# Kernel tuning notes

Measured on AMD Instinct MI355X. Metric: run time of the kernel, lower is better.

Reference implementation:

```python
import jax, jax.numpy as jnp
import numpy as np

N = 100000        # nodes
E = 3200000       # edges (avg in-degree ~32)
NG = 64           # graphs in batch
F_IN = 64         # num_node_features
AVG_LOG = float(np.log(33.0))   # avg log-degree baked from deg (avg degree 32)
BN_EPS = 1e-5
STD_EPS = 1e-5

def _glorot(key, fi, fo):
    lim = float(np.sqrt(6.0 / (fi + fo)))
    return jax.random.uniform(key, (fi, fo), jnp.float32, -lim, lim)

def setup_inputs():
    key = jax.random.key(0)
    ks = jax.random.split(key, 16)
    inp = {
        'x': jax.random.normal(ks[0], (N, F_IN), jnp.float32),
        'edge_index': jax.random.randint(ks[1], (2, E), 0, N),
        'batch': jnp.sort(jax.random.randint(ks[2], (N,), 0, NG)),
    }
    dims = [(F_IN, 96), (96, 64), (64, 32), (32, 20)]
    for i, (fi, fo) in enumerate(dims):
        inp[f'w{i}'] = _glorot(ks[3 + i], 13 * fi, fo)  # (4 aggr * 3 scalers + 1 self) * F_in
        inp[f'b{i}'] = jnp.zeros((fo,), jnp.float32)
    for i, c in enumerate([96, 64, 20]):
        inp[f'g{i}'] = jnp.ones((c,), jnp.float32)
        inp[f'be{i}'] = jnp.zeros((c,), jnp.float32)
    inp['w_lin'] = _glorot(ks[10], 20, 11)
    inp['b_lin'] = jnp.zeros((11,), jnp.float32)
    return inp

def _pna_layer(x, src, dst, cnt, degc, W, b):
    m = x[src]                                          # [E, F] gather of neighbor feats
    inv = (1.0 / degc)[:, None]
    mean = jax.ops.segment_sum(m, dst, N) * inv
    mean_sq = jax.ops.segment_sum(m * m, dst, N) * inv
    std = jnp.sqrt(jax.nn.relu(mean_sq - mean * mean) + STD_EPS)
    has = (cnt > 0)[:, None]
    mn = jnp.where(has, jax.ops.segment_min(m, dst, N), 0.0)
    mx = jnp.where(has, jax.ops.segment_max(m, dst, N), 0.0)
    agg = jnp.concatenate([mean, mn, mx, std], axis=-1)  # [N, 4F]
    logd = jnp.log(degc + 1.0)[:, None]
    out = jnp.concatenate([agg, agg * (logd / AVG_LOG), agg * (AVG_LOG / logd)], axis=-1)  # [N, 12F]
    out = jnp.concatenate([x, out], axis=-1)             # [N, 13F] self + scaled aggregations
    return out @ W + b

def _bn(x, g, b):
    mu = x.mean(0)
    var = x.var(0)  # biased var: matches torch BatchNorm training forward
    return (x - mu) * jax.lax.rsqrt(var + BN_EPS) * g + b

def _forward(x, edge_index, batch, w0, b0, w1, b1, w2, b2, w3, b3,
             g0, be0, g1, be1, g2, be2, w_lin, b_lin):
    src, dst = edge_index[0], edge_index[1]
    cnt = jax.ops.segment_sum(jnp.ones((E,), x.dtype), dst, N)  # in-degree
    degc = jnp.maximum(cnt, 1.0)
    h = jax.nn.relu(_bn(_pna_layer(x, src, dst, cnt, degc, w0, b0), g0, be0))
    h = jax.nn.relu(_bn(_pna_layer(h, src, dst, cnt, degc, w1, b1), g1, be1))
    h = jax.nn.relu(_pna_layer(h, src, dst, cnt, degc, w2, b2))
    h = _bn(_pna_layer(h, src, dst, cnt, degc, w3, b3), g2, be2)
    gcnt = jnp.maximum(jax.ops.segment_sum(jnp.ones((N,), h.dtype), batch, NG), 1.0)
    z = jax.ops.segment_sum(h, batch, NG) / gcnt[:, None]       # global mean pool [NG, 20]
    out = jax.nn.softmax(z @ w_lin + b_lin, axis=-1)            # dropout identity (eval)
    return out, z

def reference(x, edge_index, batch, w0, b0, w1, b1, w2, b2, w3, b3,
              g0, be0, g1, be1, g2, be2, w_lin, b_lin):
    return _forward(x, edge_index, batch, w0, b0, w1, b1, w2, b2, w3, b3,
                    g0, be0, g1, be1, g2, be2, w_lin, b_lin)
```

## Files before the change

kernel.cpp:

```cpp
#include <hip/hip_runtime.h>

#define NN 100000
#define NGRAPH 64
#define NPART 8
#define NPB 12500
#define DB 16
#define PW_C 2048
#define AVGLOG 3.4965075614664802f

using f32x4 = __attribute__((ext_vector_type(4))) float;
using f16x8 = __attribute__((ext_vector_type(8))) _Float16;
using f16x4 = __attribute__((ext_vector_type(4))) _Float16;
using i32x4 = __attribute__((ext_vector_type(4))) int;

__global__ __launch_bounds__(256) void k_pcnt(const int* __restrict__ ei,
                                              int* __restrict__ pcnt, int E, int W) {
  const int w = blockIdx.x * 4 + (threadIdx.x >> 6);
  const int lane = threadIdx.x & 63;
  if (w >= W) return;
  int c[NPART];
#pragma unroll
  for (int b = 0; b < NPART; ++b) c[b] = 0;
  const long long base = (long long)w * PW_C;
  for (int r = 0; r < PW_C / 256; ++r) {
    long long e0 = base + r * 256 + lane * 4;
    int bk[4] = {-1, -1, -1, -1};
    if (e0 + 3 < E) {
      i32x4 d = __builtin_nontemporal_load((const i32x4*)(ei + E + e0));
#pragma unroll
      for (int k = 0; k < 4; ++k) bk[k] = d[k] / NPB;
    } else {
#pragma unroll
      for (int k = 0; k < 4; ++k)
        if (e0 + k < E) bk[k] = ei[E + e0 + k] / NPB;
    }
#pragma unroll
    for (int b = 0; b < NPART; ++b) {
      int t = 0;
#pragma unroll
      for (int k = 0; k < 4; ++k) t += __popcll(__ballot(bk[k] == b));
      c[b] += t;
    }
  }
  if (lane == 0) {
#pragma unroll
    for (int b = 0; b < NPART; ++b) pcnt[w * NPART + b] = c[b];
  }
}

__global__ void k_pscan(const int* __restrict__ pcnt, int* __restrict__ pbase,
                        int* __restrict__ bcur, int W) {
  __shared__ int s[256];
  __shared__ int btot[NPART];
  const int t = threadIdx.x;
  const int per = (W + 255) / 256;
  for (int b = 0; b < NPART; ++b) {
    int loc = 0;
    const int w0 = t * per;
    for (int i = 0; i < per; ++i) {
      int w = w0 + i;
      if (w < W) loc += pcnt[w * NPART + b];
    }
    s[t] = loc;
    __syncthreads();
    for (int off = 1; off < 256; off <<= 1) {
      int u = (t >= off) ? s[t - off] : 0;
      __syncthreads();
      s[t] += u;
      __syncthreads();
    }
    int run = s[t] - loc;
    if (t == 255) btot[b] = s[255];
    for (int i = 0; i < per; ++i) {
      int w = w0 + i;
      if (w < W) {
        pbase[w * NPART + b] = run;
        run += pcnt[w * NPART + b];
      }
    }
    __syncthreads();
  }
  if (t < NPART) bcur[t] = btot[t];
}

__global__ __launch_bounds__(256) void k_pbin(const int* __restrict__ ei,
                                              const int* __restrict__ pbase,
                                              unsigned long long* __restrict__ bkt,
                                              int cap, int E, int W) {
  const int w = blockIdx.x * 4 + (threadIdx.x >> 6);
  const int lane = threadIdx.x & 63;
  if (w >= W) return;
  int off[NPART];
#pragma unroll
  for (int b = 0; b < NPART; ++b) off[b] = pbase[w * NPART + b];
  const unsigned long long lmask = (1ull << lane) - 1ull;
  const long long base = (long long)w * PW_C;
  for (int r = 0; r < PW_C / 256; ++r) {
    long long e0 = base + r * 256 + lane * 4;
    int bk[4] = {-1, -1, -1, -1};
    int sv[4], dv[4];
    if (e0 + 3 < E) {
      i32x4 d = __builtin_nontemporal_load((const i32x4*)(ei + E + e0));
      i32x4 s4 = __builtin_nontemporal_load((const i32x4*)(ei + e0));
#pragma unroll
      for (int k = 0; k < 4; ++k) { dv[k] = d[k]; sv[k] = s4[k]; bk[k] = d[k] / NPB; }
    } else {
#pragma unroll
      for (int k = 0; k < 4; ++k)
        if (e0 + k < E) { dv[k] = ei[E + e0 + k]; sv[k] = ei[e0 + k]; bk[k] = dv[k] / NPB; }
    }
#pragma unroll
    for (int k = 0; k < 4; ++k) {
#pragma unroll
      for (int b = 0; b < NPART; ++b) {
        unsigned long long m = __ballot(bk[k] == b);
        if (bk[k] == b) {
          int idx = off[b] + __popcll(m & lmask);
          bkt[(size_t)b * cap + idx] =
              ((unsigned long long)(unsigned)dv[k] << 32) | (unsigned)sv[k];
        }
        off[b] += __popcll(m);
      }
    }
  }
}

__global__ __launch_bounds__(256) void k_dhist(
    const unsigned long long* __restrict__ bkt, const int* __restrict__ bcur,
    int cap, int* __restrict__ dhist) {
  __shared__ int hist[NPB];
  const int p = blockIdx.x & (NPART - 1);
  const int b = blockIdx.x >> 3;
  const int tid = threadIdx.x;
  for (int i = tid; i < NPB; i += 256) hist[i] = 0;
  __syncthreads();
  const int n = bcur[p];
  const int chunk = (n + DB - 1) / DB;
  const int lo = b * chunk, hi = min(n, lo + chunk);
  const unsigned long long* base = bkt + (size_t)p * cap;
  const int plo = p * NPB;
  for (int i = lo + tid; i < hi; i += 256) {
    unsigned long long v = base[i];
    atomicAdd(&hist[(int)(v >> 32) - plo], 1);
  }
  __syncthreads();
  int* dst = dhist + ((size_t)p * DB + b) * NPB;
  for (int i = tid; i < NPB; i += 256) dst[i] = hist[i];
}

__global__ void k_mergesum(int* __restrict__ dhist, int* __restrict__ cnt,
                           int* __restrict__ bsum, int n) {
  __shared__ int s[256];
  int i = blockIdx.x * 256 + threadIdx.x;
  int acc = 0;
  if (i < n) {
    int p = i / NPB, li = i - p * NPB;
    int* hb = dhist + (size_t)p * DB * NPB + li;
#pragma unroll
    for (int b = 0; b < DB; ++b) {
      int t = hb[b * NPB];
      hb[b * NPB] = acc;
      acc += t;
    }
    cnt[i] = acc;
  }
  s[threadIdx.x] = acc;
  __syncthreads();
  for (int off = 128; off > 0; off >>= 1) {
    if (threadIdx.x < off) s[threadIdx.x] += s[threadIdx.x + off];
    __syncthreads();
  }
  if (threadIdx.x == 0) bsum[blockIdx.x] = s[0];
}

__global__ __launch_bounds__(256) void k_binfill(
    const unsigned long long* __restrict__ bkt, const int* __restrict__ bcur,
    int cap, const int* __restrict__ dhist, const int* __restrict__ row_ptr,
    int* __restrict__ colv) {
  __shared__ int rank[NPB];
  const int p = blockIdx.x & (NPART - 1);
  const int b = blockIdx.x >> 3;
  const int tid = threadIdx.x;
  const int plo = p * NPB;
  const int* soff = dhist + ((size_t)p * DB + b) * NPB;
  for (int li = tid; li < NPB; li += 256) rank[li] = row_ptr[plo + li] + soff[li];
  __syncthreads();
  const int n = bcur[p];
  const int chunk = (n + DB - 1) / DB;
  const int lo = b * chunk, hi = min(n, lo + chunk);
  const unsigned long long* base = bkt + (size_t)p * cap;
  for (int i = lo + tid; i < hi; i += 256) {
    unsigned long long v = base[i];
    int d = (int)(v >> 32);
    int s = (int)(v & 0xffffffffu);
    int pos = atomicAdd(&rank[d - plo], 1);
    colv[pos] = s;
  }
}

__global__ void k_scanb(const int* __restrict__ bsum, int* __restrict__ boff, int nb) {
  __shared__ int s[512];
  int t = threadIdx.x;
  int v = (t < nb) ? bsum[t] : 0;
  s[t] = v;
  __syncthreads();
  for (int off = 1; off < 512; off <<= 1) {
    int u = (t >= off) ? s[t - off] : 0;
    __syncthreads();
    s[t] += u;
    __syncthreads();
  }
  if (t < nb) boff[t] = s[t] - v;
}

__global__ void k_scatter(const int* __restrict__ cnt, const int* __restrict__ boff,
                          int* __restrict__ row_ptr, int n, int etot) {
  __shared__ int s[256];
  int i = blockIdx.x * 256 + threadIdx.x;
  int v = (i < n) ? cnt[i] : 0;
  s[threadIdx.x] = v;
  __syncthreads();
  for (int off = 1; off < 256; off <<= 1) {
    int u = (threadIdx.x >= off) ? s[threadIdx.x - off] : 0;
    __syncthreads();
    s[threadIdx.x] += u;
    __syncthreads();
  }
  if (i < n) row_ptr[i] = boff[blockIdx.x] + s[threadIdx.x] - v;
  if (i == 0) row_ptr[n] = etot;
}

__global__ void k_nodesc(const int* __restrict__ cnt, float* __restrict__ invd,
                         float* __restrict__ s1v, float* __restrict__ s2v, int n) {
  int i = blockIdx.x * 256 + threadIdx.x;
  if (i >= n) return;
  float degc = fmaxf((float)cnt[i], 1.f);
  invd[i] = 1.f / degc;
  float ld = logf(degc + 1.f);
  s1v[i] = ld * (1.f / AVGLOG);
  s2v[i] = AVGLOG / ld;
}

__global__ void k_wtprep(const float* __restrict__ W, _Float16* __restrict__ Wt,
                         int K, int FO, int FOP) {
  int i = blockIdx.x * 256 + threadIdx.x;
  if (i >= FOP * K) return;
  int nn = i / K, k = i - nn * K;
  float v = (nn < FO) ? W[k * FO + nn] : 0.f;
  int NT = FOP >> 4;
  int kt = k >> 5, q = (k >> 3) & 3, j = k & 7;
  int nt = nn >> 4, m = nn & 15;
  size_t idx = (((size_t)kt * NT + nt) * 64 + (q * 16 + m)) * 8 + j;
  Wt[idx] = (_Float16)v;
}

__global__ void k_xconv(const float* __restrict__ x, _Float16* __restrict__ x16, int n) {
  int i = blockIdx.x * 256 + threadIdx.x;
  if (i < n) x16[i] = (_Float16)x[i];
}

template <int F, int WPE>
__launch_bounds__(256, WPE)
__global__ void k_agg(const _Float16* __restrict__ hin, const int* __restrict__ row_ptr,
                      const int* __restrict__ colv, const float* __restrict__ invd,
                      _Float16* __restrict__ agg) {
  const int tid = threadIdx.x;
  const int r = tid >> 3, g = tid & 7;
  const int n = blockIdx.x * 32 + r;
  const int e0 = row_ptr[n], e1 = row_ptr[n + 1];
  constexpr int SEG = F / 8;
  constexpr int N8 = (SEG % 8 == 0) ? SEG / 8 : 0;
  constexpr int N4 = (SEG % 8 == 0) ? 0 : SEG / 4;
  constexpr int KTA = F / 8;
  float sm[SEG], sq[SEG], mn[SEG], mx[SEG];
  const float FINF = __builtin_inff();
#pragma unroll
  for (int j = 0; j < SEG; ++j) { sm[j] = 0.f; sq[j] = 0.f; mn[j] = FINF; mx[j] = -FINF; }
  int e = e0;
  for (; e + 1 < e1; e += 2) {
    const _Float16* ra = hin + (size_t)colv[e] * F + g * SEG;
    const _Float16* rb = hin + (size_t)colv[e + 1] * F + g * SEG;
    f16x8 a8[N8 ? N8 : 1], b8[N8 ? N8 : 1];
    f16x4 a4[N4 ? N4 : 1], b4[N4 ? N4 : 1];
    if (N8) {
#pragma unroll
      for (int c = 0; c < N8; ++c) { a8[c] = ((const f16x8*)ra)[c]; b8[c] = ((const f16x8*)rb)[c]; }
    } else {
#pragma unroll
      for (int c = 0; c < N4; ++c) { a4[c] = ((const f16x4*)ra)[c]; b4[c] = ((const f16x4*)rb)[c]; }
    }
#pragma unroll
    for (int j = 0; j < SEG; ++j) {
      float av = N8 ? (float)a8[j / 8][j % 8] : (float)a4[j / 4][j % 4];
      float bv = N8 ? (float)b8[j / 8][j % 8] : (float)b4[j / 4][j % 4];
      sm[j] += av + bv;
      sq[j] += av * av + bv * bv;
      mn[j] = fminf(mn[j], fminf(av, bv));
      mx[j] = fmaxf(mx[j], fmaxf(av, bv));
    }
  }
  if (e < e1) {
    const _Float16* ra = hin + (size_t)colv[e] * F + g * SEG;
    f16x8 a8[N8 ? N8 : 1];
    f16x4 a4[N4 ? N4 : 1];
    if (N8) {
#pragma unroll
      for (int c = 0; c < N8; ++c) a8[c] = ((const f16x8*)ra)[c];
    } else {
#pragma unroll
      for (int c = 0; c < N4; ++c) a4[c] = ((const f16x4*)ra)[c];
    }
#pragma unroll
    for (int j = 0; j < SEG; ++j) {
      float av = N8 ? (float)a8[j / 8][j % 8] : (float)a4[j / 4][j % 4];
      sm[j] += av;
      sq[j] += av * av;
      mn[j] = fminf(mn[j], av);
      mx[j] = fmaxf(mx[j], av);
    }
  }
  float iv = invd[n];
  bool has = (e1 > e0);
  const int m = n & 15;
  const size_t tb = (size_t)(n >> 4) * KTA;
#pragma unroll
  for (int c = 0; c < SEG / 4; ++c) {
    f16x4 vals[4];
#pragma unroll
    for (int l = 0; l < 4; ++l) {
      int j = 4 * c + l;
      float mean = sm[j] * iv;
      float var = sq[j] * iv - mean * mean;
      float sd = sqrtf(fmaxf(var, 0.f) + 1e-5f);
      vals[0][l] = (_Float16)mean;
      vals[1][l] = has ? (_Float16)mn[j] : (_Float16)0.f;
      vals[2][l] = has ? (_Float16)mx[j] : (_Float16)0.f;
      vals[3][l] = (_Float16)sd;
    }
    int f0 = g * SEG + 4 * c;
#pragma unroll
    for (int a = 0; a < 4; ++a) {
      int kk0 = a * F + f0;
      int kt = kk0 >> 5, q = (kk0 >> 3) & 3, j0 = kk0 & 7;
      *(f16x4*)(agg + (tb + kt) * 512 + (q * 16 + m) * 8 + j0) = vals[a];
    }
  }
}

#define MFMA16(a, b, c) __builtin_amdgcn_mfma_f32_16x16x32_f16(a, b, c, 0, 0, 0)

template <int F, int FO, int FOP, bool RELU, bool STATS, typename OT>
__launch_bounds__(256)
__global__ void k_mlp(const _Float16* __restrict__ hin, const _Float16* __restrict__ agg,
                      const float* __restrict__ s1g, const float* __restrict__ s2g,
                      const _Float16* __restrict__ Wt, const float* __restrict__ bias,
                      OT* __restrict__ hout, float* __restrict__ csum,
                      float* __restrict__ csq) {
  constexpr int F32 = F / 32;
  constexpr int KTA = F / 8;
  constexpr int NT = FOP / 16;
  constexpr int PPW = (2 * NT) / 4;
  constexpr int XW = F + 8;
  __shared__ __align__(16) _Float16 s_x[32][XW];
  __shared__ float s_cs[2][FOP];

  const int tid = threadIdx.x;
  const int n0 = blockIdx.x * 32;

  for (int idx = tid; idx < 32 * (F / 8); idx += 256) {
    int r = idx / (F / 8), c = idx % (F / 8);
    *(f16x8*)&s_x[r][8 * c] = *(const f16x8*)&hin[(size_t)(n0 + r) * F + 8 * c];
  }
  if (STATS)
    for (int u = tid; u < 2 * FOP; u += 256) (&s_cs[0][0])[u] = 0.f;
  __syncthreads();

  const int w = tid >> 6, ln = tid & 63;
  const int lm = ln & 15, q = ln >> 4;
  const int mt = w & 1;
  const int arow = mt * 16 + lm;
  f32x4 acc0[PPW], acc1[PPW], acc2[PPW];
#pragma unroll
  for (int i = 0; i < PPW; ++i)
#pragma unroll
    for (int t = 0; t < 4; ++t) { acc0[i][t] = 0.f; acc1[i][t] = 0.f; acc2[i][t] = 0.f; }

#pragma unroll
  for (int kt = 0; kt < F32; ++kt) {
    f16x8 a = *(const f16x8*)&s_x[arow][kt * 32 + 8 * q];
#pragma unroll
    for (int i = 0; i < PPW; ++i) {
      int nt = (w >> 1) + 2 * i;
      f16x8 b = *(const f16x8*)&Wt[(((size_t)kt * NT + nt) * 64 + ln) * 8];
      acc0[i] = MFMA16(a, b, acc0[i]);
    }
  }
  const size_t atb = (size_t)(blockIdx.x * 2 + mt) * KTA;
#pragma unroll
  for (int kt = 0; kt < KTA; ++kt) {
    f16x8 a = *(const f16x8*)&agg[(atb + kt) * 512 + ln * 8];
#pragma unroll
    for (int i = 0; i < PPW; ++i) {
      int nt = (w >> 1) + 2 * i;
      f16x8 b0 = *(const f16x8*)&Wt[(((size_t)(F32 + kt) * NT + nt) * 64 + ln) * 8];
      acc0[i] = MFMA16(a, b0, acc0[i]);
      f16x8 b1 = *(const f16x8*)&Wt[(((size_t)(F32 + KTA + kt) * NT + nt) * 64 + ln) * 8];
      acc1[i] = MFMA16(a, b1, acc1[i]);
      f16x8 b2 = *(const f16x8*)&Wt[(((size_t)(F32 + 2 * KTA + kt) * NT + nt) * 64 + ln) * 8];
      acc2[i] = MFMA16(a, b2, acc2[i]);
    }
  }

  float s1r[4], s2r[4];
#pragma unroll
  for (int t = 0; t < 4; ++t) {
    int node = n0 + mt * 16 + q * 4 + t;
    s1r[t] = s1g[node];
    s2r[t] = s2g[node];
  }
#pragma unroll
  for (int i = 0; i < PPW; ++i) {
    int nt = (w >> 1) + 2 * i;
    int ncol = nt * 16 + lm;
    if (FOP == FO || ncol < FO) {
      float bs = bias[ncol];
      float cs = 0.f, cq = 0.f;
#pragma unroll
      for (int t = 0; t < 4; ++t) {
        int node = n0 + mt * 16 + q * 4 + t;
        float v = acc0[i][t] + s1r[t] * acc1[i][t] + s2r[t] * acc2[i][t] + bs;
        if (RELU) v = fmaxf(v, 0.f);
        hout[(size_t)node * FO + ncol] = (OT)v;
        cs += v;
        cq += v * v;
      }
      if (STATS) {
        atomicAdd(&s_cs[0][ncol], cs);
        atomicAdd(&s_cs[1][ncol], cq);
      }
    }
  }
  if (STATS) {
    __syncthreads();
    if (tid < FO) {
      atomicAdd(&csum[tid], s_cs[0][tid]);
      atomicAdd(&csq[tid], s_cs[1][tid]);
    }
  }
}

__global__ void k_bn16(_Float16* __restrict__ h, const float* __restrict__ csum,
                       const float* __restrict__ csq, const float* __restrict__ gg,
                       const float* __restrict__ be, int n, int fo, int relu) {
  int i = blockIdx.x * 256 + threadIdx.x;
  int total = (n * fo) >> 3;
  if (i >= total) return;
  int c0 = (i << 3) % fo;
  float invn = 1.f / (float)n;
  f16x8 v = *(const f16x8*)&h[(size_t)i << 3];
  f16x8 o;
#pragma unroll
  for (int j = 0; j < 8; ++j) {
    int c = c0 + j;
    float mu = csum[c] * invn;
    float var = csq[c] * invn - mu * mu;
    float rs = rsqrtf(var + 1e-5f);
    float x = ((float)v[j] - mu) * rs * gg[c] + be[c];
    if (relu) x = fmaxf(x, 0.f);
    o[j] = (_Float16)x;
  }
  *(f16x8*)&h[(size_t)i << 3] = o;
}

__global__ void k_bnf(float* __restrict__ h, const float* __restrict__ csum,
                      const float* __restrict__ csq, const float* __restrict__ gg,
                      const float* __restrict__ be, int n, int fo, int relu) {
  int i = blockIdx.x * 256 + threadIdx.x;
  if (i >= n * fo) return;
  int c = i % fo;
  float invn = 1.f / (float)n;
  float mu = csum[c] * invn;
  float var = csq[c] * invn - mu * mu;
  float rs = rsqrtf(var + 1e-5f);
  float v = (h[i] - mu) * rs * gg[c] + be[c];
  if (relu) v = fmaxf(v, 0.f);
  h[i] = v;
}

__global__ void k_pool(const float* __restrict__ h, const int* __restrict__ batch,
                       float* __restrict__ zsum, float* __restrict__ gcnt, int n) {
  __shared__ float sv[NGRAPH * 20];
  __shared__ float sc[NGRAPH];
  int tid = threadIdx.x;
  for (int u = tid; u < NGRAPH * 20; u += 256) sv[u] = 0.f;
  if (tid < NGRAPH) sc[tid] = 0.f;
  __syncthreads();
  int i = blockIdx.x * 256 + tid;
  if (i < n) {
    int g = batch[i];
    atomicAdd(&sc[g], 1.f);
    for (int j = 0; j < 20; ++j) atomicAdd(&sv[g * 20 + j], h[(size_t)i * 20 + j]);
  }
  __syncthreads();
  if (tid < NGRAPH && sc[tid] != 0.f) {
    atomicAdd(&gcnt[tid], sc[tid]);
    for (int j = 0; j < 20; ++j) atomicAdd(&zsum[tid * 20 + j], sv[tid * 20 + j]);
  }
}

__global__ void k_head(const float* __restrict__ zsum, const float* __restrict__ gcnt,
                       const float* __restrict__ wl, const float* __restrict__ bl,
                       float* __restrict__ out) {
  int g = threadIdx.x;
  if (g >= NGRAPH) return;
  float z[20];
  float icg = 1.f / fmaxf(gcnt[g], 1.f);
#pragma unroll
  for (int j = 0; j < 20; ++j) {
    z[j] = zsum[g * 20 + j] * icg;
    out[NGRAPH * 11 + g * 20 + j] = z[j];
  }
  float lo[11];
#pragma unroll
  for (int o = 0; o < 11; ++o) {
    float a = bl[o];
    for (int j = 0; j < 20; ++j) a += z[j] * wl[j * 11 + o];
    lo[o] = a;
  }
  float m = lo[0];
  for (int o = 1; o < 11; ++o) m = fmaxf(m, lo[o]);
  float s = 0.f;
  for (int o = 0; o < 11; ++o) { lo[o] = expf(lo[o] - m); s += lo[o]; }
  float is = 1.f / s;
  for (int o = 0; o < 11; ++o) out[g * 11 + o] = lo[o] * is;
}

static inline char* carve(char*& p, size_t bytes) {
  char* r = p;
  p += (bytes + 255) & ~(size_t)255;
  return r;
}

extern "C" void kernel_launch(void* const* d_in, const int* in_sizes, int n_in,
                              void* d_out, int out_size, void* d_ws, size_t ws_size,
                              hipStream_t stream) {
  const float* x = (const float*)d_in[0];
  const int* ei = (const int*)d_in[1];
  const int* batch = (const int*)d_in[2];
  const float* W0 = (const float*)d_in[3];
  const float* b0 = (const float*)d_in[4];
  const float* W1 = (const float*)d_in[5];
  const float* b1 = (const float*)d_in[6];
  const float* W2 = (const float*)d_in[7];
  const float* b2 = (const float*)d_in[8];
  const float* W3 = (const float*)d_in[9];
  const float* b3 = (const float*)d_in[10];
  const float* g0 = (const float*)d_in[11];
  const float* be0 = (const float*)d_in[12];
  const float* g1 = (const float*)d_in[13];
  const float* be1 = (const float*)d_in[14];
  const float* g2 = (const float*)d_in[15];
  const float* be2 = (const float*)d_in[16];
  const float* wl = (const float*)d_in[17];
  const float* bl = (const float*)d_in[18];
  float* out = (float*)d_out;

  const int E = in_sizes[1] / 2;
  const int NB = (NN + 255) / 256;
  const int BCAP = E / NPART + 65536;
  const int W = (E + PW_C - 1) / PW_C;
  const int GB = (W + 3) / 4;

  char* p = (char*)d_ws;
  int* cnt = (int*)carve(p, (size_t)NN * 4);
  int* row_ptr = (int*)carve(p, (size_t)(NN + 1) * 4);
  int* bsum = (int*)carve(p, 2048);
  int* boff = (int*)carve(p, 2048);
  int* bcur = (int*)carve(p, 256);
  int* pcnt = (int*)carve(p, (size_t)W * NPART * 4);
  int* pbase = (int*)carve(p, (size_t)W * NPART * 4);
  int* colv = (int*)carve(p, (size_t)E * 4);
  unsigned long long* bkt = (unsigned long long*)carve(p, (size_t)NPART * BCAP * 8);
  int* dhist = (int*)carve(p, (size_t)NPART * DB * NPB * 4);
  float* invd = (float*)carve(p, (size_t)NN * 4);
  float* s1v = (float*)carve(p, (size_t)NN * 4);
  float* s2v = (float*)carve(p, (size_t)NN * 4);
  _Float16* Wt0 = (_Float16*)carve(p, (size_t)96 * 832 * 2);
  _Float16* Wt1 = (_Float16*)carve(p, (size_t)64 * 1248 * 2);
  _Float16* Wt2 = (_Float16*)carve(p, (size_t)32 * 832 * 2);
  _Float16* Wt3 = (_Float16*)carve(p, (size_t)32 * 416 * 2);
  float* cs = (float*)carve(p, 192 * 4);
  float* csum = cs;
  float* csq = cs + 96;
  float* pacc = (float*)carve(p, (NGRAPH * 20 + NGRAPH) * 4);
  float* zsum = pacc;
  float* gcnt = pacc + NGRAPH * 20;
  _Float16* x16 = (_Float16*)carve(p, (size_t)NN * 64 * 2);
  _Float16* hA16 = (_Float16*)carve(p, (size_t)NN * 96 * 2);
  _Float16* hB16 = (_Float16*)carve(p, (size_t)NN * 96 * 2);
  _Float16* aggb = (_Float16*)carve(p, (size_t)NN * 4 * 96 * 2);
  float* h3 = (float*)x16;

  hipMemsetAsync(pacc, 0, (NGRAPH * 20 + NGRAPH) * 4, stream);
  k_pcnt<<<GB, 256, 0, stream>>>(ei, pcnt, E, W);
  k_pscan<<<1, 256, 0, stream>>>(pcnt, pbase, bcur, W);
  k_pbin<<<GB, 256, 0, stream>>>(ei, pbase, bkt, BCAP, E, W);
  k_dhist<<<NPART * DB, 256, 0, stream>>>(bkt, bcur, BCAP, dhist);
  k_mergesum<<<NB, 256, 0, stream>>>(dhist, cnt, bsum, NN);
  k_scanb<<<1, 512, 0, stream>>>(bsum, boff, NB);
  k_scatter<<<NB, 256, 0, stream>>>(cnt, boff, row_ptr, NN, E);
  k_nodesc<<<NB, 256, 0, stream>>>(cnt, invd, s1v, s2v, NN);
  k_binfill<<<NPART * DB, 256, 0, stream>>>(bkt, bcur, BCAP, dhist, row_ptr, colv);

  k_wtprep<<<(96 * 832 + 255) / 256, 256, 0, stream>>>(W0, Wt0, 832, 96, 96);
  k_wtprep<<<(64 * 1248 + 255) / 256, 256, 0, stream>>>(W1, Wt1, 1248, 64, 64);
  k_wtprep<<<(32 * 832 + 255) / 256, 256, 0, stream>>>(W2, Wt2, 832, 32, 32);
  k_wtprep<<<(32 * 416 + 255) / 256, 256, 0, stream>>>(W3, Wt3, 416, 20, 32);
  k_xconv<<<(NN * 64 + 255) / 256, 256, 0, stream>>>(x, x16, NN * 64);

  const int GP = NN / 32;

  hipMemsetAsync(cs, 0, 192 * 4, stream);
  k_agg<64, 6><<<GP, 256, 0, stream>>>(x16, row_ptr, colv, invd, aggb);
  k_mlp<64, 96, 96, false, true, _Float16><<<GP, 256, 0, stream>>>(x16, aggb, s1v, s2v, Wt0, b0, hA16, csum, csq);
  k_bn16<<<(NN * 96 / 8 + 255) / 256, 256, 0, stream>>>(hA16, csum, csq, g0, be0, NN, 96, 1);

  hipMemsetAsync(cs, 0, 192 * 4, stream);
  k_agg<96, 4><<<GP, 256, 0, stream>>>(hA16, row_ptr, colv, invd, aggb);
  k_mlp<96, 64, 64, false, true, _Float16><<<GP, 256, 0, stream>>>(hA16, aggb, s1v, s2v, Wt1, b1, hB16, csum, csq);
  k_bn16<<<(NN * 64 / 8 + 255) / 256, 256, 0, stream>>>(hB16, csum, csq, g1, be1, NN, 64, 1);

  k_agg<64, 6><<<GP, 256, 0, stream>>>(hB16, row_ptr, colv, invd, aggb);
  k_mlp<64, 32, 32, true, false, _Float16><<<GP, 256, 0, stream>>>(hB16, aggb, s1v, s2v, Wt2, b2, hA16, csum, csq);

  hipMemsetAsync(cs, 0, 192 * 4, stream);
  k_agg<32, 8><<<GP, 256, 0, stream>>>(hA16, row_ptr, colv, invd, aggb);
  k_mlp<32, 20, 32, false, true, float><<<GP, 256, 0, stream>>>(hA16, aggb, s1v, s2v, Wt3, b3, h3, csum, csq);
  k_bnf<<<(NN * 20 + 255) / 256, 256, 0, stream>>>(h3, csum, csq, g2, be2, NN, 20, 0);

  k_pool<<<NB, 256, 0, stream>>>(h3, batch, zsum, gcnt, NN);
  k_head<<<1, 64, 0, stream>>>(zsum, gcnt, wl, bl, out);
}
```

Baseline: 895.6 us.

## Unroll gather by four, pack min/max in fp16, add nontemporal hints

The aggregation kernel now processes four neighbour edges per iteration instead of two, which puts more independent gather loads in flight. It keeps sum and sum-of-squares as packed float2 and min/max as packed half2, cutting register use and instruction count. Nontemporal hints are added to the colv loads, the agg stores and the MLP input loads so that streaming data does not crowd the gather working set out of cache. The F=96 aggregation launch bound is raised to 6 waves per EU, which risks register spilling.

Measured after the change: 948.2 us. 1.06x slower.

```diff
diff --git a/kernel.cpp b/kernel.cpp
--- a/kernel.cpp
+++ b/kernel.cpp
@@ -8,7 +8,9 @@
 #define PW_C 2048
 #define AVGLOG 3.4965075614664802f
 
+using f32x2 = __attribute__((ext_vector_type(2))) float;
 using f32x4 = __attribute__((ext_vector_type(4))) float;
+using f16x2 = __attribute__((ext_vector_type(2))) _Float16;
 using f16x8 = __attribute__((ext_vector_type(8))) _Float16;
 using f16x4 = __attribute__((ext_vector_type(4))) _Float16;
 using i32x4 = __attribute__((ext_vector_type(4))) int;
@@ -269,56 +271,73 @@
   const int n = blockIdx.x * 32 + r;
   const int e0 = row_ptr[n], e1 = row_ptr[n + 1];
   constexpr int SEG = F / 8;
-  constexpr int N8 = (SEG % 8 == 0) ? SEG / 8 : 0;
-  constexpr int N4 = (SEG % 8 == 0) ? 0 : SEG / 4;
+  constexpr int NP = SEG / 2;
   constexpr int KTA = F / 8;
-  float sm[SEG], sq[SEG], mn[SEG], mx[SEG];
-  const float FINF = __builtin_inff();
-#pragma unroll
-  for (int j = 0; j < SEG; ++j) { sm[j] = 0.f; sq[j] = 0.f; mn[j] = FINF; mx[j] = -FINF; }
+  f32x2 sm[NP], sq[NP];
+  f16x2 mn[NP], mx[NP];
+  const _Float16 HPI = __builtin_bit_cast(_Float16, (unsigned short)0x7C00);
+  const _Float16 HNI = __builtin_bit_cast(_Float16, (unsigned short)0xFC00);
+#pragma unroll
+  for (int p = 0; p < NP; ++p) {
+    sm[p] = (f32x2){0.f, 0.f};
+    sq[p] = (f32x2){0.f, 0.f};
+    mn[p] = (f16x2){HPI, HPI};
+    mx[p] = (f16x2){HNI, HNI};
+  }
+
+  auto loadrow = [&](const _Float16* ra, f16x2* pr) {
+    if constexpr (SEG % 8 == 0) {
+#pragma unroll
+      for (int c = 0; c < SEG / 8; ++c) {
+        f16x8 v = ((const f16x8*)ra)[c];
+        pr[4 * c + 0] = (f16x2){v[0], v[1]};
+        pr[4 * c + 1] = (f16x2){v[2], v[3]};
+        pr[4 * c + 2] = (f16x2){v[4], v[5]};
+        pr[4 * c + 3] = (f16x2){v[6], v[7]};
+      }
+    } else {
+#pragma unroll
+      for (int c = 0; c < SEG / 4; ++c) {
+        f16x4 v = ((const f16x4*)ra)[c];
+        pr[2 * c + 0] = (f16x2){v[0], v[1]};
+        pr[2 * c + 1] = (f16x2){v[2], v[3]};
+      }
+    }
+  };
+  auto accum = [&](const f16x2* pr) {
+#pragma unroll
+    for (int p = 0; p < NP; ++p) {
+      f32x2 f = __builtin_convertvector(pr[p], f32x2);
+      sm[p] += f;
+      sq[p] += f * f;
+      mn[p] = __builtin_elementwise_min(mn[p], pr[p]);
+      mx[p] = __builtin_elementwise_max(mx[p], pr[p]);
+    }
+  };
+
   int e = e0;
-  for (; e + 1 < e1; e += 2) {
-    const _Float16* ra = hin + (size_t)colv[e] * F + g * SEG;
-    const _Float16* rb = hin + (size_t)colv[e + 1] * F + g * SEG;
-    f16x8 a8[N8 ? N8 : 1], b8[N8 ? N8 : 1];
-    f16x4 a4[N4 ? N4 : 1], b4[N4 ? N4 : 1];
-    if (N8) {
-#pragma unroll
-      for (int c = 0; c < N8; ++c) { a8[c] = ((const f16x8*)ra)[c]; b8[c] = ((const f16x8*)rb)[c]; }
-    } else {
-#pragma unroll
-      for (int c = 0; c < N4; ++c) { a4[c] = ((const f16x4*)ra)[c]; b4[c] = ((const f16x4*)rb)[c]; }
-    }
-#pragma unroll
-    for (int j = 0; j < SEG; ++j) {
-      float av = N8 ? (float)a8[j / 8][j % 8] : (float)a4[j / 4][j % 4];
-      float bv = N8 ? (float)b8[j / 8][j % 8] : (float)b4[j / 4][j % 4];
-      sm[j] += av + bv;
-      sq[j] += av * av + bv * bv;
-      mn[j] = fminf(mn[j], fminf(av, bv));
-      mx[j] = fmaxf(mx[j], fmaxf(av, bv));
-    }
-  }
-  if (e < e1) {
-    const _Float16* ra = hin + (size_t)colv[e] * F + g * SEG;
-    f16x8 a8[N8 ? N8 : 1];
-    f16x4 a4[N4 ? N4 : 1];
-    if (N8) {
-#pragma unroll
-      for (int c = 0; c < N8; ++c) a8[c] = ((const f16x8*)ra)[c];
-    } else {
-#pragma unroll
-      for (int c = 0; c < N4; ++c) a4[c] = ((const f16x4*)ra)[c];
-    }
-#pragma unroll
-    for (int j = 0; j < SEG; ++j) {
-      float av = N8 ? (float)a8[j / 8][j % 8] : (float)a4[j / 4][j % 4];
-      sm[j] += av;
-      sq[j] += av * av;
-      mn[j] = fminf(mn[j], av);
-      mx[j] = fmaxf(mx[j], av);
-    }
-  }
+  for (; e + 3 < e1; e += 4) {
+    int c0 = __builtin_nontemporal_load(&colv[e + 0]);
+    int c1 = __builtin_nontemporal_load(&colv[e + 1]);
+    int c2 = __builtin_nontemporal_load(&colv[e + 2]);
+    int c3 = __builtin_nontemporal_load(&colv[e + 3]);
+    f16x2 r0[NP], r1[NP], r2[NP], r3[NP];
+    loadrow(hin + (size_t)c0 * F + g * SEG, r0);
+    loadrow(hin + (size_t)c1 * F + g * SEG, r1);
+    loadrow(hin + (size_t)c2 * F + g * SEG, r2);
+    loadrow(hin + (size_t)c3 * F + g * SEG, r3);
+    accum(r0);
+    accum(r1);
+    accum(r2);
+    accum(r3);
+  }
+  for (; e < e1; ++e) {
+    int c0 = __builtin_nontemporal_load(&colv[e]);
+    f16x2 r0[NP];
+    loadrow(hin + (size_t)c0 * F + g * SEG, r0);
+    accum(r0);
+  }
+
   float iv = invd[n];
   bool has = (e1 > e0);
   const int m = n & 15;
@@ -329,12 +348,13 @@
 #pragma unroll
     for (int l = 0; l < 4; ++l) {
       int j = 4 * c + l;
-      float mean = sm[j] * iv;
-      float var = sq[j] * iv - mean * mean;
+      int p = j >> 1, k = j & 1;
+      float mean = sm[p][k] * iv;
+      float var = sq[p][k] * iv - mean * mean;
       float sd = sqrtf(fmaxf(var, 0.f) + 1e-5f);
       vals[0][l] = (_Float16)mean;
-      vals[1][l] = has ? (_Float16)mn[j] : (_Float16)0.f;
-      vals[2][l] = has ? (_Float16)mx[j] : (_Float16)0.f;
+      vals[1][l] = has ? mn[p][k] : (_Float16)0.f;
+      vals[2][l] = has ? mx[p][k] : (_Float16)0.f;
       vals[3][l] = (_Float16)sd;
     }
     int f0 = g * SEG + 4 * c;
@@ -342,7 +362,8 @@
     for (int a = 0; a < 4; ++a) {
       int kk0 = a * F + f0;
       int kt = kk0 >> 5, q = (kk0 >> 3) & 3, j0 = kk0 & 7;
-      *(f16x4*)(agg + (tb + kt) * 512 + (q * 16 + m) * 8 + j0) = vals[a];
+      __builtin_nontemporal_store(vals[a],
+          (f16x4*)(agg + (tb + kt) * 512 + (q * 16 + m) * 8 + j0));
     }
   }
 }
@@ -369,7 +390,8 @@
 
   for (int idx = tid; idx < 32 * (F / 8); idx += 256) {
     int r = idx / (F / 8), c = idx % (F / 8);
-    *(f16x8*)&s_x[r][8 * c] = *(const f16x8*)&hin[(size_t)(n0 + r) * F + 8 * c];
+    *(f16x8*)&s_x[r][8 * c] =
+        __builtin_nontemporal_load((const f16x8*)&hin[(size_t)(n0 + r) * F + 8 * c]);
   }
   if (STATS)
     for (int u = tid; u < 2 * FOP; u += 256) (&s_cs[0][0])[u] = 0.f;
@@ -398,7 +420,7 @@
   const size_t atb = (size_t)(blockIdx.x * 2 + mt) * KTA;
 #pragma unroll
   for (int kt = 0; kt < KTA; ++kt) {
-    f16x8 a = *(const f16x8*)&agg[(atb + kt) * 512 + ln * 8];
+    f16x8 a = __builtin_nontemporal_load((const f16x8*)&agg[(atb + kt) * 512 + ln * 8]);
 #pragma unroll
     for (int i = 0; i < PPW; ++i) {
       int nt = (w >> 1) + 2 * i;
@@ -626,7 +648,7 @@
   k_bn16<<<(NN * 96 / 8 + 255) / 256, 256, 0, stream>>>(hA16, csum, csq, g0, be0, NN, 96, 1);
 
   hipMemsetAsync(cs, 0, 192 * 4, stream);
-  k_agg<96, 4><<<GP, 256, 0, stream>>>(hA16, row_ptr, colv, invd, aggb);
+  k_agg<96, 6><<<GP, 256, 0, stream>>>(hA16, row_ptr, colv, invd, aggb);
   k_mlp<96, 64, 64, false, true, _Float16><<<GP, 256, 0, stream>>>(hA16, aggb, s1v, s2v, Wt1, b1, hB16, csum, csq);
   k_bn16<<<(NN * 64 / 8 + 255) / 256, 256, 0, stream>>>(hB16, csum, csq, g1, be1, NN, 64, 1);
 
```
